# Optimization experiments

Measured on AMD Instinct MI355X. Metric: run time of the kernel, lower is better.

The kernel has to match this reference:

```python
import jax, jax.numpy as jnp
import numpy as np

BN_EPS = 1e-5


def setup_inputs() -> dict:
    key = jax.random.key(0)
    ks = jax.random.split(key, 5)
    B, T, N, C, O, K, E = 2, 4, 50000, 32, 32, 3, 800000
    x = jax.random.normal(ks[0], (B, T, N, C), dtype=jnp.float32)
    edge_index = jax.random.randint(ks[1], (2, E), 0, N, dtype=jnp.int64)
    edge_weight = jax.random.uniform(ks[2], (E,), dtype=jnp.float32)
    W = jax.random.normal(ks[3], (K, C, O), dtype=jnp.float32) * 0.05
    bias = jnp.zeros((O,), dtype=jnp.float32)
    gamma = jnp.ones((O,), dtype=jnp.float32)
    beta = jnp.zeros((O,), dtype=jnp.float32)
    return {"x": x, "edge_index": edge_index, "edge_weight": edge_weight,
            "W": W, "bias": bias, "gamma": gamma, "beta": beta}


def reference(x, edge_index, edge_weight, W, bias, gamma, beta):
    # x: [B, T, N, C]; edge_index: [2, E]; W: [K, C, O]
    B, T, N, C = x.shape
    K = W.shape[0]
    src, dst = edge_index[0], edge_index[1]

    # Scaled Laplacian L_hat = 2L/lambda_max - I with sym norm, lambda_max=2
    # => L_hat = -D^{-1/2} A D^{-1/2} (zero diagonal), PyG ChebConv default.
    deg = jax.ops.segment_sum(edge_weight, src, num_segments=N)
    safe = jnp.where(deg > 0, deg, 1.0)
    dinv = jnp.where(deg > 0, 1.0 / jnp.sqrt(safe), 0.0)
    norm = -dinv[src] * edge_weight * dinv[dst]  # [E]

    # Batch all (b, t) slices together: [N, M, C] with M = B*T
    xn = jnp.transpose(x, (2, 0, 1, 3)).reshape(N, B * T, C)

    def lap(z):  # sparse SpMM applied to every (b,t) slice at once
        return jax.ops.segment_sum(norm[:, None, None] * z[src], dst,
                                   num_segments=N)

    # Chebyshev recursion: T0 = x, T1 = L_hat x, Tk = 2 L_hat T_{k-1} - T_{k-2}
    Tx_prev2 = xn
    out = jnp.einsum('nmc,co->nmo', Tx_prev2, W[0])
    if K > 1:
        Tx_prev = lap(xn)
        out = out + jnp.einsum('nmc,co->nmo', Tx_prev, W[1])
        for k in range(2, K):
            Tx_k = 2.0 * lap(Tx_prev) - Tx_prev2
            out = out + jnp.einsum('nmc,co->nmo', Tx_k, W[k])
            Tx_prev2, Tx_prev = Tx_prev, Tx_k
    out = out + bias  # [N, M, O]

    # BatchNorm1d in training mode, applied per (b,t) slice over nodes,
    # exactly as the original per-slice loop does (biased variance).
    mean = jnp.mean(out, axis=0, keepdims=True)              # [1, M, O]
    var = jnp.mean((out - mean) ** 2, axis=0, keepdims=True)  # [1, M, O]
    y = gamma * (out - mean) * jax.lax.rsqrt(var + BN_EPS) + beta
    y = jax.nn.relu(y)

    return jnp.transpose(y.reshape(N, B, T, -1), (1, 2, 0, 3))  # [B,T,N,O]
```

## Files before the change

### kernel.cpp

```cpp
#include <hip/hip_runtime.h>

#define NNODES 50000
#define NEDGES 800000
#define MB 8
#define CF 32
#define OF 32
#define FPN 256
#define TOTAL_OUT (MB * NNODES * OF)

#define BSH 9
#define BINW 512
#define NB ((NNODES + BINW - 1) / BINW)
#define PH (NB * 2)
#define NBA 1024
#define EPB ((NEDGES + NBA - 1) / NBA)
#define CAPL 20
#define LBW 24
#define CH 8
#define BINCAP 13312
#define STCAP 7936

typedef unsigned short ushort_t;
typedef unsigned int uint_t;
typedef __attribute__((ext_vector_type(8))) short bf16x8;
typedef __attribute__((ext_vector_type(4))) float f32x4;

__device__ __forceinline__ ushort_t f2bf(float f) {
    uint_t u = __float_as_uint(f);
    u += 0x7FFFu + ((u >> 16) & 1u);
    return (ushort_t)(u >> 16);
}
__device__ __forceinline__ float bflo(uint_t u) { return __uint_as_float(u << 16); }
__device__ __forceinline__ float bfhi(uint_t u) { return __uint_as_float(u & 0xFFFF0000u); }

__device__ __forceinline__ bool detect_is64(const int* ei) {
    int lane = threadIdx.x & 63;
    int v = ei[2 * lane + 1];
    return __ballot(v != 0) == 0ULL;
}

__global__ void __launch_bounds__(256) k_init(const float* __restrict__ W,
                                              ushort_t* __restrict__ wbf,
                                              int* __restrict__ g_cntD,
                                              int* __restrict__ g_cntS,
                                              float* __restrict__ stats) {
    int t = threadIdx.x;
    if (t < NB) { g_cntD[t] = 0; g_cntS[t] = 0; }
    stats[t] = 0.0f;
    stats[256 + t] = 0.0f;
    for (int i = t; i < 384; i += 256) {
        int k    = i >> 7;
        int rem  = i & 127;
        int oh   = rem >> 6;
        int lane = rem & 63;
        int quad = lane >> 4;
        int colc = lane & 15;
        ushort_t* d = wbf + (size_t)i * 8;
        for (int j = 0; j < 8; j++) {
            int c = quad * 8 + j;
            int o = oh * 16 + colc;
            d[j] = f2bf(W[k * (CF * OF) + c * OF + o]);
        }
    }
}

__global__ void __launch_bounds__(256) k_build(const int* __restrict__ ei,
                                               const float* __restrict__ w,
                                               const float* __restrict__ x,
                                               int* __restrict__ g_cntD,
                                               int* __restrict__ g_cntS,
                                               int2* __restrict__ binD,
                                               int2* __restrict__ binS,
                                               ushort_t* __restrict__ xn) {
    int blk = blockIdx.x;
    int t = threadIdx.x;
    __shared__ int l_cnt[NB];
    __shared__ int l_base[NB];
    __shared__ ushort_t l_pfx[NB + 1];
    __shared__ int2 l_buf[NB][LBW];
    if (blk < NBA) {
        bool is64 = detect_is64(ei);
        const int2* ei2 = (const int2*)ei;
        for (int i = t; i < NB; i += 256) l_cnt[i] = 0;
        __syncthreads();
        int e0 = blk * EPB;
        int e1 = min(e0 + EPB, NEDGES);
        int sreg[4];
        float wreg[4];
        #pragma unroll
        for (int i = 0; i < 4; i++) {
            int e = e0 + t + i * 256;
            bool ok = (e < e1);
            int s = 0, d = 0;
            float wt = 0.0f;
            if (ok) {
                if (is64) {
                    s = ei2[e].x;
                    d = ei2[NEDGES + e].x;
                } else {
                    s = ei[e];
                    d = ei[NEDGES + e];
                }
                wt = w[e];
            }
            sreg[i] = ok ? s : -1;
            wreg[i] = wt;
            if (ok) {
                int bin = d >> BSH;
                int2 entry;
                entry.x = s | ((d & (BINW - 1)) << 16);
                entry.y = __float_as_int(wt);
                int pos = atomicAdd(&l_cnt[bin], 1);
                if (pos < CAPL) {
                    l_buf[bin][pos] = entry;
                } else {
                    int gp = atomicAdd(&g_cntD[bin], 1);
                    if (gp < BINCAP) binD[(size_t)bin * BINCAP + gp] = entry;
                }
            }
        }
        __syncthreads();
        if (t < NB) {
            int c = min(l_cnt[t], CAPL);
            int p = (c + CH - 1) & ~(CH - 1);
            for (int i = c; i < p; i++) l_buf[t][i] = make_int2(0, 0);
            l_cnt[t] = p;
            if (p > 0) l_base[t] = atomicAdd(&g_cntD[t], p);
        }
        __syncthreads();
        if (t == 0) {
            int sacc = 0;
            for (int b2 = 0; b2 < NB; b2++) {
                l_pfx[b2] = (ushort_t)sacc;
                sacc += l_cnt[b2];
            }
            l_pfx[NB] = (ushort_t)sacc;
        }
        __syncthreads();
        {
            int total = l_pfx[NB];
            for (int idx = t; idx < total; idx += 256) {
                int lo = 0, hi = NB - 1;
                while (lo < hi) {
                    int mid = (lo + hi + 1) >> 1;
                    if ((int)l_pfx[mid] <= idx) lo = mid; else hi = mid - 1;
                }
                int rel = idx - (int)l_pfx[lo];
                int gp = l_base[lo] + rel;
                if (gp < BINCAP) binD[(size_t)lo * BINCAP + gp] = l_buf[lo][rel];
            }
        }
        __syncthreads();
        for (int i = t; i < NB; i += 256) l_cnt[i] = 0;
        __syncthreads();
        #pragma unroll
        for (int i = 0; i < 4; i++) {
            if (sreg[i] >= 0) {
                int s = sreg[i];
                int bin = s >> BSH;
                int2 entry;
                entry.x = s & (BINW - 1);
                entry.y = __float_as_int(wreg[i]);
                int pos = atomicAdd(&l_cnt[bin], 1);
                if (pos < CAPL) {
                    l_buf[bin][pos] = entry;
                } else {
                    int gp = atomicAdd(&g_cntS[bin], 1);
                    if (gp < BINCAP) binS[(size_t)bin * BINCAP + gp] = entry;
                }
            }
        }
        __syncthreads();
        if (t < NB) {
            int c = min(l_cnt[t], CAPL);
            int p = (c + CH - 1) & ~(CH - 1);
            for (int i = c; i < p; i++) l_buf[t][i] = make_int2(0, 0);
            l_cnt[t] = p;
            if (p > 0) l_base[t] = atomicAdd(&g_cntS[t], p);
        }
        __syncthreads();
        if (t == 0) {
            int sacc = 0;
            for (int b2 = 0; b2 < NB; b2++) {
                l_pfx[b2] = (ushort_t)sacc;
                sacc += l_cnt[b2];
            }
            l_pfx[NB] = (ushort_t)sacc;
        }
        __syncthreads();
        {
            int total = l_pfx[NB];
            for (int idx = t; idx < total; idx += 256) {
                int lo = 0, hi = NB - 1;
                while (lo < hi) {
                    int mid = (lo + hi + 1) >> 1;
                    if ((int)l_pfx[mid] <= idx) lo = mid; else hi = mid - 1;
                }
                int rel = idx - (int)l_pfx[lo];
                int gp = l_base[lo] + rel;
                if (gp < BINCAP) binS[(size_t)lo * BINCAP + gp] = l_buf[lo][rel];
            }
        }
    } else {
        int bb = blk - NBA;
        int lane = t & 63;
        int n = bb * 4 + (t >> 6);
        int m = lane >> 3;
        int c = (4 * lane) & 31;
        const float4 v = *(const float4*)(x + ((size_t)m * NNODES + n) * CF + c);
        uint2 d;
        d.x = (uint_t)f2bf(v.x) | ((uint_t)f2bf(v.y) << 16);
        d.y = (uint_t)f2bf(v.z) | ((uint_t)f2bf(v.w) << 16);
        *(uint2*)(xn + (size_t)n * FPN + 4 * lane) = d;
    }
}

__global__ void __launch_bounds__(256) k_prep(const int* __restrict__ g_cntD,
                                              const int* __restrict__ g_cntS,
                                              const int2* __restrict__ binD,
                                              const int2* __restrict__ binS,
                                              float* __restrict__ dinv,
                                              int2* __restrict__ csr,
                                              int* __restrict__ csr_off) {
    __shared__ int2 l_stage[STCAP];
    __shared__ int l_h[256];
    __shared__ int l_end[256];
    __shared__ int l_ws[4];
    int b = blockIdx.x;
    int t = threadIdx.x;
    if (b < NB) {
        float* l_acc = (float*)l_stage;
        l_acc[t] = 0.0f;
        l_acc[t + 256] = 0.0f;
        __syncthreads();
        int cnt = min(g_cntS[b], BINCAP);
        const int2* bp = binS + (size_t)b * BINCAP;
        for (int i = t; i < cnt; i += 256) {
            int2 e = bp[i];
            atomicAdd(&l_acc[e.x], __int_as_float(e.y));
        }
        __syncthreads();
        #pragma unroll
        for (int i = 0; i < 2; i++) {
            int idx = i * 256 + t;
            int n = b * BINW + idx;
            if (n < NNODES) {
                float s = l_acc[idx];
                dinv[n] = (s > 0.0f) ? (1.0f / sqrtf(s)) : 0.0f;
            }
        }
        return;
    }
    int b2 = b - NB;
    int bin = b2 >> 1, h = b2 & 1;
    int lane = t & 63, wv = t >> 6;

    l_h[t] = 0;
    __syncthreads();
    int cnt = min(g_cntD[bin], BINCAP);
    const int2* bp = binD + (size_t)bin * BINCAP;
    for (int i = t; i < cnt; i += 256) {
        int2 e = bp[i];
        int dl = e.x >> 16;
        if (e.y != 0 && (dl >> 8) == h) atomicAdd(&l_h[dl & 255], 1);
    }
    __syncthreads();

    int hreal = l_h[t];
    int ppad = min((hreal + 15) & ~15, 64);
    int v = ppad;
    #pragma unroll
    for (int off = 1; off < 64; off <<= 1) {
        int u = __shfl_up(v, off);
        if (lane >= off) v += u;
    }
    if (lane == 63) l_ws[wv] = v;
    __syncthreads();
    int wpre = 0;
    for (int i = 0; i < wv; i++) wpre += l_ws[i];
    int excl = wpre + v - ppad;
    int tot = l_ws[0] + l_ws[1] + l_ws[2] + l_ws[3];
    int ztot = min(tot, STCAP);

    int n = bin * BINW + h * 256 + t;
    if (n < NNODES) csr_off[n] = ((b2 * STCAP + excl) << 3) | (ppad >> 4);
    l_h[t] = excl;
    l_end[t] = min(excl + ppad, STCAP);
    __syncthreads();

    for (int i = t; i < ztot; i += 256) l_stage[i] = make_int2(0, 0);
    __syncthreads();
    for (int i = t; i < cnt; i += 256) {
        int2 e = bp[i];
        int dl = e.x >> 16;
        if (e.y != 0 && (dl >> 8) == h) {
            int node = dl & 255;
            int slot = atomicAdd(&l_h[node], 1);
            if (slot < l_end[node]) l_stage[slot] = make_int2(e.x & 0xFFFF, e.y);
        }
    }
    __syncthreads();

    for (int i = t; i < ztot; i += 256) csr[(size_t)b2 * STCAP + i] = l_stage[i];
}

__global__ void __launch_bounds__(256) k_spmm1(const ushort_t* __restrict__ xn,
                                               const int* __restrict__ csr_off,
                                               const int2* __restrict__ csr,
                                               const float* __restrict__ dinv,
                                               ushort_t* __restrict__ t1) {
    int t = threadIdx.x;
    int lane = t & 63;
    int n = __builtin_amdgcn_readfirstlane(blockIdx.x * 4 + (t >> 6));
    int pk = csr_off[n];
    int off = pk >> 3;
    int cnt = (pk & 7) << 4;
    float dn = dinv[n];
    float a0 = 0.0f, a1 = 0.0f, a2 = 0.0f, a3 = 0.0f;
    if (cnt > 0) {
        int j = off + min(lane, cnt - 1);
        int2 ed = csr[j];
        int cv = ed.x;
        float vw = -dinv[cv] * __int_as_float(ed.y) * dn;
        uint_t vv = __float_as_uint(vw);
        for (int k = 0; k < cnt; k += 16) {
            int sc[16]; float v[16];
            #pragma unroll
            for (int i = 0; i < 16; i++) {
                sc[i] = __builtin_amdgcn_readlane(cv, k + i);
                v[i] = __uint_as_float(__builtin_amdgcn_readlane((int)vv, k + i));
            }
            uint2 u[16];
            #pragma unroll
            for (int i = 0; i < 16; i++)
                u[i] = *(const uint2*)(xn + (size_t)sc[i] * FPN + 4 * lane);
            #pragma unroll
            for (int i = 0; i < 16; i++) {
                a0 += v[i] * bflo(u[i].x);
                a1 += v[i] * bfhi(u[i].x);
                a2 += v[i] * bflo(u[i].y);
                a3 += v[i] * bfhi(u[i].y);
            }
        }
    }
    uint2 d;
    d.x = (uint_t)f2bf(a0) | ((uint_t)f2bf(a1) << 16);
    d.y = (uint_t)f2bf(a2) | ((uint_t)f2bf(a3) << 16);
    *(uint2*)(t1 + (size_t)n * FPN + 4 * lane) = d;
}

__global__ void __launch_bounds__(256) k_spmm2w(const ushort_t* __restrict__ t1,
                                                const ushort_t* __restrict__ xn0,
                                                const int* __restrict__ csr_off,
                                                const int2* __restrict__ csr,
                                                const float* __restrict__ dinv,
                                                const ushort_t* __restrict__ wbf,
                                                const float* __restrict__ bias,
                                                float* __restrict__ out) {
    __shared__ ushort_t lds_t2[16][264];
    int t = threadIdx.x;
    int lane = t & 63;
    int wv = t >> 6;
    int n0 = blockIdx.x * 16;
    for (int q = 0; q < 4; q++) {
        int n = __builtin_amdgcn_readfirstlane(n0 + wv * 4 + q);
        int pk = csr_off[n];
        int off = pk >> 3;
        int cnt = (pk & 7) << 4;
        float dn = dinv[n];
        float a0 = 0.0f, a1 = 0.0f, a2 = 0.0f, a3 = 0.0f;
        if (cnt > 0) {
            int j = off + min(lane, cnt - 1);
            int2 ed = csr[j];
            int cv = ed.x;
            float vw = -dinv[cv] * __int_as_float(ed.y) * dn;
            uint_t vv = __float_as_uint(vw);
            for (int k = 0; k < cnt; k += 16) {
                int sc[16]; float v[16];
                #pragma unroll
                for (int i = 0; i < 16; i++) {
                    sc[i] = __builtin_amdgcn_readlane(cv, k + i);
                    v[i] = __uint_as_float(__builtin_amdgcn_readlane((int)vv, k + i));
                }
                uint2 u[16];
                #pragma unroll
                for (int i = 0; i < 16; i++)
                    u[i] = *(const uint2*)(t1 + (size_t)sc[i] * FPN + 4 * lane);
                #pragma unroll
                for (int i = 0; i < 16; i++) {
                    a0 += v[i] * bflo(u[i].x);
                    a1 += v[i] * bfhi(u[i].x);
                    a2 += v[i] * bflo(u[i].y);
                    a3 += v[i] * bfhi(u[i].y);
                }
            }
        }
        const uint2 xu = *(const uint2*)(xn0 + (size_t)n * FPN + 4 * lane);
        a0 = 2.0f * a0 - bflo(xu.x);
        a1 = 2.0f * a1 - bfhi(xu.x);
        a2 = 2.0f * a2 - bflo(xu.y);
        a3 = 2.0f * a3 - bfhi(xu.y);
        uint2 d;
        d.x = (uint_t)f2bf(a0) | ((uint_t)f2bf(a1) << 16);
        d.y = (uint_t)f2bf(a2) | ((uint_t)f2bf(a3) << 16);
        *(uint2*)&lds_t2[wv * 4 + q][4 * lane] = d;
    }
    __syncthreads();
    int quad = lane >> 4, col = lane & 15;
    bf16x8 B[6];
    #pragma unroll
    for (int i = 0; i < 6; i++)
        B[i] = *(const bf16x8*)(wbf + (size_t)(i * 64 + lane) * 8);
    float blo = bias[col], bhi = bias[16 + col];
    size_t aoff = (size_t)(n0 + col) * FPN + quad * 8;
    #pragma unroll
    for (int mi = 0; mi < 2; mi++) {
        int m = wv * 2 + mi;
        bf16x8 A0 = *(const bf16x8*)(xn0 + aoff + m * 32);
        bf16x8 A1 = *(const bf16x8*)(t1 + aoff + m * 32);
        bf16x8 A2 = *(const bf16x8*)&lds_t2[col][quad * 8 + m * 32];
        f32x4 lo = { blo, blo, blo, blo };
        f32x4 hi = { bhi, bhi, bhi, bhi };
        lo = __builtin_amdgcn_mfma_f32_16x16x32_bf16(A0, B[0], lo, 0, 0, 0);
        hi = __builtin_amdgcn_mfma_f32_16x16x32_bf16(A0, B[1], hi, 0, 0, 0);
        lo = __builtin_amdgcn_mfma_f32_16x16x32_bf16(A1, B[2], lo, 0, 0, 0);
        hi = __builtin_amdgcn_mfma_f32_16x16x32_bf16(A1, B[3], hi, 0, 0, 0);
        lo = __builtin_amdgcn_mfma_f32_16x16x32_bf16(A2, B[4], lo, 0, 0, 0);
        hi = __builtin_amdgcn_mfma_f32_16x16x32_bf16(A2, B[5], hi, 0, 0, 0);
        float* ob = out + ((size_t)m * NNODES + n0 + quad * 4) * OF + col;
        #pragma unroll
        for (int r = 0; r < 4; r++) {
            ob[(size_t)r * OF]      = lo[r];
            ob[(size_t)r * OF + 16] = hi[r];
        }
    }
}

__global__ void __launch_bounds__(256) k_stats(const float* __restrict__ out,
                                               float* __restrict__ stats) {
    int m = blockIdx.y;
    int t = threadIdx.x;
    int o4 = t & 7, row = t >> 3;
    int n0 = blockIdx.x * 1024;
    int nend = min(n0 + 1024, NNODES);
    float sx = 0, sy = 0, sz = 0, sw = 0;
    float qx = 0, qy = 0, qz = 0, qw = 0;
    for (int n = n0 + row; n < nend; n += 32) {
        const float4 v = *(const float4*)(out + ((size_t)m * NNODES + n) * OF + o4 * 4);
        sx += v.x; sy += v.y; sz += v.z; sw += v.w;
        qx += v.x * v.x; qy += v.y * v.y; qz += v.z * v.z; qw += v.w * v.w;
    }
    __shared__ float4 sS[256];
    __shared__ float4 sQ[256];
    sS[t] = make_float4(sx, sy, sz, sw);
    sQ[t] = make_float4(qx, qy, qz, qw);
    __syncthreads();
    for (int off = 16; off >= 1; off >>= 1) {
        if (row < off) {
            float4 a = sS[t], b = sS[t + off * 8];
            sS[t] = make_float4(a.x + b.x, a.y + b.y, a.z + b.z, a.w + b.w);
            float4 c = sQ[t], d = sQ[t + off * 8];
            sQ[t] = make_float4(c.x + d.x, c.y + d.y, c.z + d.z, c.w + d.w);
        }
        __syncthreads();
    }
    if (row == 0) {
        float4 s = sS[t], q = sQ[t];
        int base = m * 32 + o4 * 4;
        atomicAdd(&stats[base + 0], s.x);
        atomicAdd(&stats[base + 1], s.y);
        atomicAdd(&stats[base + 2], s.z);
        atomicAdd(&stats[base + 3], s.w);
        atomicAdd(&stats[256 + base + 0], q.x);
        atomicAdd(&stats[256 + base + 1], q.y);
        atomicAdd(&stats[256 + base + 2], q.z);
        atomicAdd(&stats[256 + base + 3], q.w);
    }
}

__global__ void __launch_bounds__(256) k_final(float* __restrict__ out,
                                               const float* __restrict__ stats,
                                               const float* __restrict__ gamma,
                                               const float* __restrict__ beta) {
    int idx4 = blockIdx.x * 256 + threadIdx.x;
    size_t base = (size_t)idx4 * 4;
    int o = (int)(base & 31);
    int m = (int)(base / ((size_t)NNODES * OF));
    int mo = m * 32 + o;
    const float4 sm = *(const float4*)(stats + mo);
    const float4 sq = *(const float4*)(stats + 256 + mo);
    const float4 g  = *(const float4*)(gamma + o);
    const float4 bt = *(const float4*)(beta + o);
    const float inv_n = 1.0f / (float)NNODES;
    float4 v = *(const float4*)(out + base);
    {
        float mean = sm.x * inv_n, var = sq.x * inv_n - mean * mean;
        float sc = g.x * rsqrtf(var + 1e-5f);
        v.x = fmaxf(v.x * sc + (bt.x - sc * mean), 0.0f);
    }
    {
        float mean = sm.y * inv_n, var = sq.y * inv_n - mean * mean;
        float sc = g.y * rsqrtf(var + 1e-5f);
        v.y = fmaxf(v.y * sc + (bt.y - sc * mean), 0.0f);
    }
    {
        float mean = sm.z * inv_n, var = sq.z * inv_n - mean * mean;
        float sc = g.z * rsqrtf(var + 1e-5f);
        v.z = fmaxf(v.z * sc + (bt.z - sc * mean), 0.0f);
    }
    {
        float mean = sm.w * inv_n, var = sq.w * inv_n - mean * mean;
        float sc = g.w * rsqrtf(var + 1e-5f);
        v.w = fmaxf(v.w * sc + (bt.w - sc * mean), 0.0f);
    }
    *(float4*)(out + base) = v;
}

extern "C" void kernel_launch(void* const* d_in, const int* in_sizes, int n_in,
                              void* d_out, int out_size, void* d_ws, size_t ws_size,
                              hipStream_t stream) {
    const float* x     = (const float*)d_in[0];
    const int*   ei    = (const int*)d_in[1];
    const float* w     = (const float*)d_in[2];
    const float* W     = (const float*)d_in[3];
    const float* bias  = (const float*)d_in[4];
    const float* gamma = (const float*)d_in[5];
    const float* beta  = (const float*)d_in[6];
    float* out = (float*)d_out;

    char* p = (char*)d_ws;
    auto alloc = [&](size_t bytes) {
        char* r = p;
        p += (bytes + 511) & ~(size_t)511;
        return r;
    };
    int*      g_cntD  = (int*)alloc((size_t)NB * 4);
    int*      g_cntS  = (int*)alloc((size_t)NB * 4);
    float*    stats   = (float*)alloc(512 * 4);
    float*    dinv    = (float*)alloc((size_t)NNODES * 4);
    int2*     binD    = (int2*)alloc((size_t)NB * BINCAP * 8);
    int2*     binS    = (int2*)alloc((size_t)NB * BINCAP * 8);
    int2*     csr     = (int2*)alloc((size_t)PH * STCAP * 8);
    int*      csr_off = (int*)alloc((size_t)(NNODES + 1) * 4);
    ushort_t* wbf     = (ushort_t*)alloc(384 * 8 * 2);
    ushort_t* xn      = (ushort_t*)alloc((size_t)NNODES * FPN * 2);
    ushort_t* t1      = (ushort_t*)alloc((size_t)NNODES * FPN * 2);

    k_init<<<1, 256, 0, stream>>>(W, wbf, g_cntD, g_cntS, stats);
    k_build<<<NBA + NNODES / 4, 256, 0, stream>>>(ei, w, x, g_cntD, g_cntS,
                                                  binD, binS, xn);
    k_prep<<<NB + PH, 256, 0, stream>>>(g_cntD, g_cntS, binD, binS,
                                        dinv, csr, csr_off);
    k_spmm1<<<NNODES / 4, 256, 0, stream>>>(xn, csr_off, csr, dinv, t1);
    k_spmm2w<<<NNODES / 16, 256, 0, stream>>>(t1, xn, csr_off, csr, dinv,
                                              wbf, bias, out);
    dim3 sgrid((NNODES + 1023) / 1024, MB);
    k_stats<<<sgrid, 256, 0, stream>>>(out, stats);
    k_final<<<TOTAL_OUT / 4 / 256, 256, 0, stream>>>(out, stats, gamma, beta);
}
```

Before: 334.0 us.

## Fuse back-half kernels into one persistent cooperative kernel with grid syncs

Replaces the four separate launches (spmm1, spmm2 plus weight multiply, stats, final BN/ReLU) with a single persistent cooperative kernel. The stages are separated by grid-wide syncs and work is distributed over grid-stride loops. The intent is to remove launch gaps and tail effects between the kernels and to hoist the weight and bias loads once per block. The trade-off is that the grid is capped by occupancy, which may limit parallelism in the gather-heavy SpMM stages, and that grid.sync adds its own overhead; the old kernels remain as a fallback.

New measurement: 789.4 us. 2.36x slower.

```diff
diff --git a/kernel.cpp b/kernel.cpp
--- a/kernel.cpp
+++ b/kernel.cpp
@@ -1,4 +1,7 @@
 #include <hip/hip_runtime.h>
+#include <hip/hip_cooperative_groups.h>
+
+namespace cg = cooperative_groups;
 
 #define NNODES 50000
 #define NEDGES 800000
@@ -19,6 +22,9 @@
 #define CH 8
 #define BINCAP 13312
 #define STCAP 7936
+#define NCHUNK ((NNODES + 1023) / 1024)
+#define SJOBS (NCHUNK * MB)
+#define FJOBS (TOTAL_OUT / 4 / 256)
 
 typedef unsigned short ushort_t;
 typedef unsigned int uint_t;
@@ -300,18 +306,14 @@
         }
     }
     __syncthreads();
-
     for (int i = t; i < ztot; i += 256) csr[(size_t)b2 * STCAP + i] = l_stage[i];
 }
 
-__global__ void __launch_bounds__(256) k_spmm1(const ushort_t* __restrict__ xn,
-                                               const int* __restrict__ csr_off,
-                                               const int2* __restrict__ csr,
-                                               const float* __restrict__ dinv,
-                                               ushort_t* __restrict__ t1) {
-    int t = threadIdx.x;
-    int lane = t & 63;
-    int n = __builtin_amdgcn_readfirstlane(blockIdx.x * 4 + (t >> 6));
+
+__device__ __forceinline__ void spmm1_node(int n, int lane,
+        const ushort_t* __restrict__ xn, const int* __restrict__ csr_off,
+        const int2* __restrict__ csr, const float* __restrict__ dinv,
+        ushort_t* __restrict__ t1) {
     int pk = csr_off[n];
     int off = pk >> 3;
     int cnt = (pk & 7) << 4;
@@ -349,19 +351,11 @@
     *(uint2*)(t1 + (size_t)n * FPN + 4 * lane) = d;
 }
 
-__global__ void __launch_bounds__(256) k_spmm2w(const ushort_t* __restrict__ t1,
-                                                const ushort_t* __restrict__ xn0,
-                                                const int* __restrict__ csr_off,
-                                                const int2* __restrict__ csr,
-                                                const float* __restrict__ dinv,
-                                                const ushort_t* __restrict__ wbf,
-                                                const float* __restrict__ bias,
-                                                float* __restrict__ out) {
-    __shared__ ushort_t lds_t2[16][264];
-    int t = threadIdx.x;
-    int lane = t & 63;
-    int wv = t >> 6;
-    int n0 = blockIdx.x * 16;
+__device__ __forceinline__ void spmm2w_tile(int n0, int lane, int wv,
+        const ushort_t* __restrict__ t1, const ushort_t* __restrict__ xn,
+        const int* __restrict__ csr_off, const int2* __restrict__ csr,
+        const float* __restrict__ dinv, const bf16x8* B, float blo, float bhi,
+        float* __restrict__ out, ushort_t (*lds_t2)[264]) {
     for (int q = 0; q < 4; q++) {
         int n = __builtin_amdgcn_readfirstlane(n0 + wv * 4 + q);
         int pk = csr_off[n];
@@ -395,7 +389,7 @@
                 }
             }
         }
-        const uint2 xu = *(const uint2*)(xn0 + (size_t)n * FPN + 4 * lane);
+        const uint2 xu = *(const uint2*)(xn + (size_t)n * FPN + 4 * lane);
         a0 = 2.0f * a0 - bflo(xu.x);
         a1 = 2.0f * a1 - bfhi(xu.x);
         a2 = 2.0f * a2 - bflo(xu.y);
@@ -407,16 +401,11 @@
     }
     __syncthreads();
     int quad = lane >> 4, col = lane & 15;
-    bf16x8 B[6];
-    #pragma unroll
-    for (int i = 0; i < 6; i++)
-        B[i] = *(const bf16x8*)(wbf + (size_t)(i * 64 + lane) * 8);
-    float blo = bias[col], bhi = bias[16 + col];
     size_t aoff = (size_t)(n0 + col) * FPN + quad * 8;
     #pragma unroll
     for (int mi = 0; mi < 2; mi++) {
         int m = wv * 2 + mi;
-        bf16x8 A0 = *(const bf16x8*)(xn0 + aoff + m * 32);
+        bf16x8 A0 = *(const bf16x8*)(xn + aoff + m * 32);
         bf16x8 A1 = *(const bf16x8*)(t1 + aoff + m * 32);
         bf16x8 A2 = *(const bf16x8*)&lds_t2[col][quad * 8 + m * 32];
         f32x4 lo = { blo, blo, blo, blo };
@@ -434,14 +423,17 @@
             ob[(size_t)r * OF + 16] = hi[r];
         }
     }
-}
-
-__global__ void __launch_bounds__(256) k_stats(const float* __restrict__ out,
-                                               float* __restrict__ stats) {
-    int m = blockIdx.y;
-    int t = threadIdx.x;
+    __syncthreads();
+}
+
+__device__ __forceinline__ void stats_job(int job, int t,
+        const float* __restrict__ out, float* __restrict__ stats,
+        float4* sS) {
+    float4* sQ = sS + 256;
+    int m = job / NCHUNK;
+    int nb = job % NCHUNK;
     int o4 = t & 7, row = t >> 3;
-    int n0 = blockIdx.x * 1024;
+    int n0 = nb * 1024;
     int nend = min(n0 + 1024, NNODES);
     float sx = 0, sy = 0, sz = 0, sw = 0;
     float qx = 0, qy = 0, qz = 0, qw = 0;
@@ -450,8 +442,6 @@
         sx += v.x; sy += v.y; sz += v.z; sw += v.w;
         qx += v.x * v.x; qy += v.y * v.y; qz += v.z * v.z; qw += v.w * v.w;
     }
-    __shared__ float4 sS[256];
-    __shared__ float4 sQ[256];
     sS[t] = make_float4(sx, sy, sz, sw);
     sQ[t] = make_float4(qx, qy, qz, qw);
     __syncthreads();
@@ -478,11 +468,10 @@
     }
 }
 
-__global__ void __launch_bounds__(256) k_final(float* __restrict__ out,
-                                               const float* __restrict__ stats,
-                                               const float* __restrict__ gamma,
-                                               const float* __restrict__ beta) {
-    int idx4 = blockIdx.x * 256 + threadIdx.x;
+__device__ __forceinline__ void final_job(int job, int t,
+        float* __restrict__ out, const float* __restrict__ stats,
+        const float* __restrict__ gamma, const float* __restrict__ beta) {
+    int idx4 = job * 256 + t;
     size_t base = (size_t)idx4 * 4;
     int o = (int)(base & 31);
     int m = (int)(base / ((size_t)NNODES * OF));
@@ -514,6 +503,97 @@
         v.w = fmaxf(v.w * sc + (bt.w - sc * mean), 0.0f);
     }
     *(float4*)(out + base) = v;
+}
+
+__global__ void __launch_bounds__(256, 4)
+k_back(const ushort_t* __restrict__ xn, ushort_t* __restrict__ t1,
+       const int* __restrict__ csr_off, const int2* __restrict__ csr,
+       const float* __restrict__ dinv, const ushort_t* __restrict__ wbf,
+       const float* __restrict__ bias, float* __restrict__ out,
+       float* __restrict__ stats, const float* __restrict__ gamma,
+       const float* __restrict__ beta) {
+    cg::grid_group grid = cg::this_grid();
+    __shared__ __align__(16) ushort_t lds_t2[16][264];
+    int t = threadIdx.x;
+    int lane = t & 63;
+    int wv = t >> 6;
+
+    for (int tile = blockIdx.x; tile < NNODES / 4; tile += gridDim.x) {
+        int n = __builtin_amdgcn_readfirstlane(tile * 4 + wv);
+        spmm1_node(n, lane, xn, csr_off, csr, dinv, t1);
+    }
+    __threadfence();
+    grid.sync();
+    __threadfence();
+
+    {
+        bf16x8 B[6];
+        #pragma unroll
+        for (int i = 0; i < 6; i++)
+            B[i] = *(const bf16x8*)(wbf + (size_t)(i * 64 + lane) * 8);
+        int col = lane & 15;
+        float blo = bias[col], bhi = bias[16 + col];
+        for (int tile = blockIdx.x; tile < NNODES / 16; tile += gridDim.x)
+            spmm2w_tile(tile * 16, lane, wv, t1, xn, csr_off, csr, dinv,
+                        B, blo, bhi, out, lds_t2);
+    }
+    __threadfence();
+    grid.sync();
+    __threadfence();
+
+    for (int job = blockIdx.x; job < SJOBS; job += gridDim.x)
+        stats_job(job, t, out, stats, (float4*)&lds_t2[0][0]);
+    __threadfence();
+    grid.sync();
+    __threadfence();
+
+    for (int job = blockIdx.x; job < FJOBS; job += gridDim.x)
+        final_job(job, t, out, stats, gamma, beta);
+}
+
+__global__ void __launch_bounds__(256) k_spmm1(const ushort_t* __restrict__ xn,
+                                               const int* __restrict__ csr_off,
+                                               const int2* __restrict__ csr,
+                                               const float* __restrict__ dinv,
+                                               ushort_t* __restrict__ t1) {
+    int t = threadIdx.x;
+    int n = __builtin_amdgcn_readfirstlane(blockIdx.x * 4 + (t >> 6));
+    spmm1_node(n, t & 63, xn, csr_off, csr, dinv, t1);
+}
+
+__global__ void __launch_bounds__(256) k_spmm2w(const ushort_t* __restrict__ t1,
+                                                const ushort_t* __restrict__ xn,
+                                                const int* __restrict__ csr_off,
+                                                const int2* __restrict__ csr,
+                                                const float* __restrict__ dinv,
+                                                const ushort_t* __restrict__ wbf,
+                                                const float* __restrict__ bias,
+                                                float* __restrict__ out) {
+    __shared__ __align__(16) ushort_t lds_t2[16][264];
+    int t = threadIdx.x;
+    int lane = t & 63;
+    int wv = t >> 6;
+    bf16x8 B[6];
+    #pragma unroll
+    for (int i = 0; i < 6; i++)
+        B[i] = *(const bf16x8*)(wbf + (size_t)(i * 64 + lane) * 8);
+    int col = lane & 15;
+    float blo = bias[col], bhi = bias[16 + col];
+    spmm2w_tile(blockIdx.x * 16, lane, wv, t1, xn, csr_off, csr, dinv,
+                B, blo, bhi, out, lds_t2);
+}
+
+__global__ void __launch_bounds__(256) k_stats(const float* __restrict__ out,
+                                               float* __restrict__ stats) {
+    __shared__ __align__(16) float4 sbuf[512];
+    stats_job(blockIdx.y * NCHUNK + blockIdx.x, threadIdx.x, out, stats, sbuf);
+}
+
+__global__ void __launch_bounds__(256) k_final(float* __restrict__ out,
+                                               const float* __restrict__ stats,
+                                               const float* __restrict__ gamma,
+                                               const float* __restrict__ beta) {
+    final_job(blockIdx.x, threadIdx.x, out, stats, gamma, beta);
 }
 
 extern "C" void kernel_launch(void* const* d_in, const int* in_sizes, int n_in,
@@ -551,10 +631,32 @@
                                                   binD, binS, xn);
     k_prep<<<NB + PH, 256, 0, stream>>>(g_cntD, g_cntS, binD, binS,
                                         dinv, csr, csr_off);
-    k_spmm1<<<NNODES / 4, 256, 0, stream>>>(xn, csr_off, csr, dinv, t1);
-    k_spmm2w<<<NNODES / 16, 256, 0, stream>>>(t1, xn, csr_off, csr, dinv,
-                                              wbf, bias, out);
-    dim3 sgrid((NNODES + 1023) / 1024, MB);
-    k_stats<<<sgrid, 256, 0, stream>>>(out, stats);
-    k_final<<<TOTAL_OUT / 4 / 256, 256, 0, stream>>>(out, stats, gamma, beta);
-}
+
+    bool done = false;
+    int nbk = 0;
+    if (hipOccupancyMaxActiveBlocksPerMultiprocessor(
+            &nbk, (const void*)k_back, 256, 0) == hipSuccess && nbk >= 1) {
+        int grid = nbk * 256;
+        if (grid > 2048) grid = 2048;
+        const ushort_t* xn_c = xn;
+        const int* csr_off_c = csr_off;
+        const int2* csr_c = csr;
+        const float* dinv_c = dinv;
+        const ushort_t* wbf_c = wbf;
+        void* args[] = { (void*)&xn_c, (void*)&t1, (void*)&csr_off_c,
+                         (void*)&csr_c, (void*)&dinv_c, (void*)&wbf_c,
+                         (void*)&bias, (void*)&out, (void*)&stats,
+                         (void*)&gamma, (void*)&beta };
+        if (hipLaunchCooperativeKernel((void*)k_back, dim3(grid), dim3(256),
+                                       args, 0, stream) == hipSuccess)
+            done = true;
+    }
+    if (!done) {
+        k_spmm1<<<NNODES / 4, 256, 0, stream>>>(xn, csr_off, csr, dinv, t1);
+        k_spmm2w<<<NNODES / 16, 256, 0, stream>>>(t1, xn, csr_off, csr, dinv,
+                                                  wbf, bias, out);
+        dim3 sgrid(NCHUNK, MB);
+        k_stats<<<sgrid, 256, 0, stream>>>(out, stats);
+        k_final<<<FJOBS, 256, 0, stream>>>(out, stats, gamma, beta);
+    }
+}
```

## Fuse BatchNorm statistics accumulation into SpMM/MFMA epilogue, drop stats kernel

Applied to the files above, without the earlier changes.

Computes per-channel sum and sum-of-squares directly from MFMA accumulators in k_spmm2w using wave shuffles and global atomics, removing the separate k_stats kernel. This avoids re-reading the full fp32 output and one launch. In exchange it issues many more float atomics onto 512 addresses, which may contend heavily.

After: 351.5 us. 5.3% more time.

```diff
diff --git a/kernel.cpp b/kernel.cpp
--- a/kernel.cpp
+++ b/kernel.cpp
@@ -300,7 +300,6 @@
         }
     }
     __syncthreads();
-
     for (int i = t; i < ztot; i += 256) csr[(size_t)b2 * STCAP + i] = l_stage[i];
 }
 
@@ -356,8 +355,9 @@
                                                 const float* __restrict__ dinv,
                                                 const ushort_t* __restrict__ wbf,
                                                 const float* __restrict__ bias,
-                                                float* __restrict__ out) {
-    __shared__ ushort_t lds_t2[16][264];
+                                                float* __restrict__ out,
+                                                float* __restrict__ stats) {
+    __shared__ __align__(16) ushort_t lds_t2[16][264];
     int t = threadIdx.x;
     int lane = t & 63;
     int wv = t >> 6;
@@ -433,48 +433,20 @@
             ob[(size_t)r * OF]      = lo[r];
             ob[(size_t)r * OF + 16] = hi[r];
         }
-    }
-}
-
-__global__ void __launch_bounds__(256) k_stats(const float* __restrict__ out,
-                                               float* __restrict__ stats) {
-    int m = blockIdx.y;
-    int t = threadIdx.x;
-    int o4 = t & 7, row = t >> 3;
-    int n0 = blockIdx.x * 1024;
-    int nend = min(n0 + 1024, NNODES);
-    float sx = 0, sy = 0, sz = 0, sw = 0;
-    float qx = 0, qy = 0, qz = 0, qw = 0;
-    for (int n = n0 + row; n < nend; n += 32) {
-        const float4 v = *(const float4*)(out + ((size_t)m * NNODES + n) * OF + o4 * 4);
-        sx += v.x; sy += v.y; sz += v.z; sw += v.w;
-        qx += v.x * v.x; qy += v.y * v.y; qz += v.z * v.z; qw += v.w * v.w;
-    }
-    __shared__ float4 sS[256];
-    __shared__ float4 sQ[256];
-    sS[t] = make_float4(sx, sy, sz, sw);
-    sQ[t] = make_float4(qx, qy, qz, qw);
-    __syncthreads();
-    for (int off = 16; off >= 1; off >>= 1) {
-        if (row < off) {
-            float4 a = sS[t], b = sS[t + off * 8];
-            sS[t] = make_float4(a.x + b.x, a.y + b.y, a.z + b.z, a.w + b.w);
-            float4 c = sQ[t], d = sQ[t + off * 8];
-            sQ[t] = make_float4(c.x + d.x, c.y + d.y, c.z + d.z, c.w + d.w);
-        }
-        __syncthreads();
-    }
-    if (row == 0) {
-        float4 s = sS[t], q = sQ[t];
-        int base = m * 32 + o4 * 4;
-        atomicAdd(&stats[base + 0], s.x);
-        atomicAdd(&stats[base + 1], s.y);
-        atomicAdd(&stats[base + 2], s.z);
-        atomicAdd(&stats[base + 3], s.w);
-        atomicAdd(&stats[256 + base + 0], q.x);
-        atomicAdd(&stats[256 + base + 1], q.y);
-        atomicAdd(&stats[256 + base + 2], q.z);
-        atomicAdd(&stats[256 + base + 3], q.w);
+        float s0 = lo[0] + lo[1] + lo[2] + lo[3];
+        float q0 = lo[0]*lo[0] + lo[1]*lo[1] + lo[2]*lo[2] + lo[3]*lo[3];
+        float s1 = hi[0] + hi[1] + hi[2] + hi[3];
+        float q1 = hi[0]*hi[0] + hi[1]*hi[1] + hi[2]*hi[2] + hi[3]*hi[3];
+        s0 += __shfl_xor(s0, 16); s0 += __shfl_xor(s0, 32);
+        q0 += __shfl_xor(q0, 16); q0 += __shfl_xor(q0, 32);
+        s1 += __shfl_xor(s1, 16); s1 += __shfl_xor(s1, 32);
+        q1 += __shfl_xor(q1, 16); q1 += __shfl_xor(q1, 32);
+        if (lane < 16) {
+            atomicAdd(&stats[m * 32 + lane], s0);
+            atomicAdd(&stats[256 + m * 32 + lane], q0);
+            atomicAdd(&stats[m * 32 + 16 + lane], s1);
+            atomicAdd(&stats[256 + m * 32 + 16 + lane], q1);
+        }
     }
 }
 
@@ -553,8 +525,6 @@
                                         dinv, csr, csr_off);
     k_spmm1<<<NNODES / 4, 256, 0, stream>>>(xn, csr_off, csr, dinv, t1);
     k_spmm2w<<<NNODES / 16, 256, 0, stream>>>(t1, xn, csr_off, csr, dinv,
-                                              wbf, bias, out);
-    dim3 sgrid((NNODES + 1023) / 1024, MB);
-    k_stats<<<sgrid, 256, 0, stream>>>(out, stats);
+                                              wbf, bias, out, stats);
     k_final<<<TOTAL_OUT / 4 / 256, 256, 0, stream>>>(out, stats, gamma, beta);
 }
```
